# Optimization experiments

Hardware: AMD Instinct MI355X
Metric: run time of the kernel (lower is better)

The kernel has to match this reference:

```python
import jax, jax.numpy as jnp
import numpy as np

TAU = 0.01          # init_temperature
N_CODEWORDS = 512
EPS = 1e-10


def setup_inputs() -> dict:
    key = jax.random.key(0)
    k1, k2, k3 = jax.random.split(key, 3)
    B, C, H, W = 8, 256, 64, 64
    K = N_CODEWORDS
    feats = jax.random.normal(k1, (B, C, H, W), dtype=jnp.float32)
    codebook = jax.random.normal(k2, (K, C), dtype=jnp.float32)
    # standard Gumbel(0,1) noise, matching torch's F.gumbel_softmax sampling
    gumbel_noise = jax.random.gumbel(k3, (B, H * W, K), dtype=jnp.float32)
    return {"feats": feats, "codebook": codebook, "gumbel_noise": gumbel_noise}


def reference(feats, codebook, gumbel_noise):
    B, C, H, W = feats.shape
    K = codebook.shape[0]
    N = H * W
    # (B, C, H, W) -> (B, N, C) tokens
    f = feats.reshape(B, C, N).transpose(0, 2, 1)
    # affinity[b,n,k] = ((f[b,n,:] - cb[k,:]).sum(-1))**2
    # sum over channels commutes with the subtraction, so reduce first
    # instead of materializing the (B, N, K, C) broadcast the torch code builds.
    sf = f.sum(axis=-1)            # (B, N)
    sw = codebook.sum(axis=-1)     # (K,)
    affinity = (sf[:, :, None] - sw[None, None, :]) ** 2   # (B, N, K)
    logits = jnp.exp(-affinity)
    # gumbel-softmax (soft, hard=False), tau = TAU, over codeword axis
    soft_one_hot = jax.nn.softmax((logits + gumbel_noise) / TAU, axis=2)
    qy = jax.nn.softmax(logits, axis=2)
    kld_loss = jnp.sum(qy * jnp.log(qy * K + EPS), axis=2).mean()
    codewords = jnp.argmax(soft_one_hot, axis=2).reshape(B, H, W)
    # weighted codeword sum: (B, N, K) @ (K, C) -> (B, N, C)
    sel = jnp.einsum("bnk,kc->bnc", soft_one_hot, codebook)
    sel_codewords = sel.transpose(0, 2, 1).reshape(B, C, H, W)
    mat_id_probs = soft_one_hot.transpose(0, 2, 1).reshape(B, K, H, W)
    return (sel_codewords, codewords, kld_loss, mat_id_probs)
```

## Files before the change

### kernel.cpp

```cpp
#include <hip/hip_runtime.h>
#include <math.h>
#include <stdint.h>

#define NB  8
#define NC  256
#define NHW 4096
#define NK  512

#define OFF_SEL 0ULL
#define OFF_CW  8388608ULL
#define OFF_KLD 8421376ULL
#define OFF_MAT 8421377ULL
#define MAT_COUNT 16777216ULL
#define OUT_TOTAL (OFF_MAT + MAT_COUNT)

typedef float f4v __attribute__((ext_vector_type(4)));


template <int C>
__device__ __forceinline__ float fdpp(float x) {
    return __int_as_float(__builtin_amdgcn_update_dpp(0, __float_as_int(x), C, 0xF, 0xF, true));
}
template <int C>
__device__ __forceinline__ int idpp(int x) {
    return __builtin_amdgcn_update_dpp(0, x, C, 0xF, 0xF, true);
}
__device__ __forceinline__ float fswz16(float x) {
    return __int_as_float(__builtin_amdgcn_ds_swizzle(__float_as_int(x), 0x401F));
}
__device__ __forceinline__ int iswz16(int x) {
    return __builtin_amdgcn_ds_swizzle(x, 0x401F);
}

__global__ void gumbel_prep(const float* __restrict__ cb, double* __restrict__ ws) {
    const int l = threadIdx.x & 63;
    const int w = threadIdx.x >> 6;
    const int k = blockIdx.x * 4 + w;
    const float4 v = *reinterpret_cast<const float4*>(cb + (size_t)k * NC + l * 4);
    double s = (double)v.x + (double)v.y + (double)v.z + (double)v.w;
    #pragma unroll
    for (int off = 32; off > 0; off >>= 1) s += __shfl_xor(s, off);
    if (l == 0) ws[k] = s;
    if (blockIdx.x == 0 && threadIdx.x == 0) ws[NK] = 0.0;
}

__global__ void zmat(float* __restrict__ out) {
    const size_t base4 = 2105345ULL;
    const size_t n4    = 4194303ULL;
    size_t i = (size_t)blockIdx.x * blockDim.x + threadIdx.x;
    const size_t stride = (size_t)gridDim.x * blockDim.x;
    f4v* o4 = reinterpret_cast<f4v*>(out) + base4;
    const f4v z = {0.f, 0.f, 0.f, 0.f};
    for (; i < n4; i += stride) __builtin_nontemporal_store(z, o4 + i);
    if (blockIdx.x == 0 && threadIdx.x < 4) {
        out[OFF_MAT + threadIdx.x] = 0.f;
        if (threadIdx.x == 0) out[OUT_TOTAL - 1] = 0.f;
    }
}

__global__ void __launch_bounds__(512, 4)
gs_main(const float* __restrict__ feats, const float* __restrict__ gumbel,
        const float* __restrict__ cb, double* __restrict__ ws,
        float* __restrict__ out) {
    __shared__ double part[8][64];
    __shared__ float  sw_f[NK];
    __shared__ double sf_d[64];
    __shared__ float  sf_f[64];
    __shared__ int    kcnt[64];
    __shared__ int    klist[64][25];
    __shared__ float  wlist[64][25];
    __shared__ double kldp[8];

    const int tid = threadIdx.x;
    const int l   = tid & 63;
    const int w   = tid >> 6;
    const int b   = blockIdx.x >> 6;
    const int n0  = (blockIdx.x & 63) * 64;

    {
        const float* fp = feats + ((size_t)b * NC + w * 32) * NHW + n0 + l;
        double s = 0.0;
        #pragma unroll
        for (int i = 0; i < 32; ++i) s += (double)fp[(size_t)i * NHW];
        part[w][l] = s;
        sw_f[tid] = (float)ws[tid];
        __syncthreads();
        if (tid < 64) {
            double a = 0.0;
            #pragma unroll
            for (int i = 0; i < 8; ++i) a += part[i][tid];
            sf_d[tid] = a; sf_f[tid] = (float)a;
            kcnt[tid] = 0;
        }
        __syncthreads();
    }

    float swreg[8];
    #pragma unroll
    for (int jj = 0; jj < 8; ++jj) swreg[jj] = sw_f[l + 64 * jj];

    double kld_wave = 0.0;
    float gc[8], gn[8];
    {
        const float* gp = gumbel + ((size_t)(b * NHW) + n0 + w * 8) * NK;
        #pragma unroll
        for (int jj = 0; jj < 8; ++jj) gc[jj] = gp[l + 64 * jj];
    }
    #pragma unroll
    for (int i = 0; i < 8; ++i) {
        const int tt = w * 8 + i;
        const int n  = n0 + tt;
        if (i < 7) {
            const float* gpn = gumbel + ((size_t)(b * NHW) + n + 1) * NK;
            #pragma unroll
            for (int jj = 0; jj < 8; ++jj) gn[jj] = gpn[l + 64 * jj];
        }
        const float sft = sf_f[tt];
        float y[8];
        float M = -1.0e30f, YS = -1.0e30f; int KB = 0;
        float E = 0.f, T = 0.f;
        #pragma unroll
        for (int jj = 0; jj < 8; ++jj) {
            const int k = l + 64 * jj;
            const float d = sft - swreg[jj];
            const float logit = __expf(-d * d);
            const float yy = logit + gc[jj];
            y[jj] = yy;
            const float h = fmaf(logit, fmaf(logit, fmaf(logit, fmaf(logit,
                              1.f/120.f, 1.f/24.f), 1.f/6.f), 0.5f), 1.f);
            const float xh = logit * h;
            E += xh;
            T = fmaf(logit, 1.f + xh, T);
            if (yy > M) { YS = M; M = yy; KB = k; }
            else YS = fmaxf(YS, yy);
        }
        #define BSTEP(GF, GI) { \
            const float oM = GF(M); const int oK = GI(KB); \
            const float oY = GF(YS); const float oE = GF(E); const float oT = GF(T); \
            const float nys = fmaxf(fmaxf(YS, oY), fminf(M, oM)); \
            if (oM > M || (oM == M && oK < KB)) { M = oM; KB = oK; } \
            YS = nys; E += oE; T += oT; }
        BSTEP(fdpp<0xB1>,  idpp<0xB1>)
        BSTEP(fdpp<0x4E>,  idpp<0x4E>)
        BSTEP(fdpp<0x141>, idpp<0x141>)
        BSTEP(fdpp<0x140>, idpp<0x140>)
        BSTEP(fswz16,      iswz16)
        #define SH32F(x) __shfl_xor(x, 32)
        #define SH32I(x) __shfl_xor(x, 32)
        BSTEP(SH32F, SH32I)
        #undef SH32F
        #undef SH32I
        #undef BSTEP
        E += 512.f;

        if (M - YS < 5e-3f) {
            const double sfd = sf_d[tt];
            double ym64 = -1.0e300; int kb64 = 0;
            #pragma unroll
            for (int jj = 0; jj < 8; ++jj) {
                const int k = l + 64 * jj;
                const double dd = sfd - ws[k];
                const double aff = dd * dd;
                const double lg = (aff < 45.0) ? exp(-aff) : 0.0;
                const double yy = lg + (double)gc[jj];
                if (yy > ym64) { ym64 = yy; kb64 = k; }
            }
            #pragma unroll
            for (int off = 1; off < 64; off <<= 1) {
                const double oy = __shfl_xor(ym64, off);
                const int    ok = __shfl_xor(kb64, off);
                if (oy > ym64 || (oy == ym64 && ok < kb64)) { ym64 = oy; kb64 = ok; }
            }
            KB = kb64;
        }
        if (l == 0) {
            out[OFF_CW + (size_t)b * NHW + n] = (float)KB;
            kld_wave += (double)(T / E + 6.2383246250395075f - logf(E));
        }

        const float thrM = M - 0.17f;
        #pragma unroll
        for (int jj = 0; jj < 8; ++jj) {
            if (y[jj] > thrM) {
                const float p = __expf((y[jj] - M) * 100.0f);
                const int idx = atomicAdd(&kcnt[tt], 1);
                if (idx < 24) { klist[tt][idx] = l + 64 * jj; wlist[tt][idx] = p; }
            }
        }
        #pragma unroll
        for (int jj = 0; jj < 8; ++jj) gc[jj] = gn[jj];
    }
    if (l == 0) kldp[w] = kld_wave;
    __syncthreads();
    if (tid == 0) {
        double acc = 0.0;
        #pragma unroll
        for (int i = 0; i < 8; ++i) acc += kldp[i];
        atomicAdd(&ws[NK], acc);
    }

    if (tid < 64) {
        const int cnt = min(kcnt[tid], 24);
        float S = 0.f;
        for (int e = 0; e < cnt; ++e) S += wlist[tid][e];
        const float inv = 1.f / S;
        float* orow = out + OFF_MAT + ((size_t)b * NK) * NHW + n0 + tid;
        for (int e = 0; e < cnt; ++e) {
            const float wgt = wlist[tid][e] * inv;
            wlist[tid][e] = wgt;
            orow[(size_t)klist[tid][e] * NHW] = wgt;
        }
        kcnt[tid] = cnt;
    }
    __syncthreads();

    {
        const int cnt = kcnt[l];
        #pragma unroll
        for (int half = 0; half < 2; ++half) {
            float acc[16];
            #pragma unroll
            for (int i2 = 0; i2 < 16; ++i2) acc[i2] = 0.f;
            for (int e = 0; e < cnt; ++e) {
                const int k = klist[l][e];
                const float wgt = wlist[l][e];
                const float4* cr = reinterpret_cast<const float4*>(
                    cb + (size_t)k * NC + w * 32 + half * 16);
                #pragma unroll
                for (int q = 0; q < 4; ++q) {
                    const float4 v = cr[q];
                    acc[q * 4 + 0] += wgt * v.x; acc[q * 4 + 1] += wgt * v.y;
                    acc[q * 4 + 2] += wgt * v.z; acc[q * 4 + 3] += wgt * v.w;
                }
            }
            float* basep = out + OFF_SEL + ((size_t)b * NC + w * 32 + half * 16) * NHW + n0 + l;
            #pragma unroll
            for (int i2 = 0; i2 < 16; ++i2)
                __builtin_nontemporal_store(acc[i2], basep + (size_t)i2 * NHW);
        }
    }
}

__global__ void gumbel_fin(const double* __restrict__ ws, float* __restrict__ out) {
    out[OFF_KLD] = (float)(ws[NK] * (1.0 / 32768.0));
}

extern "C" void kernel_launch(void* const* d_in, const int* in_sizes, int n_in,
                              void* d_out, int out_size, void* d_ws, size_t ws_size,
                              hipStream_t stream) {
    const float* feats = (const float*)d_in[0];
    const float* cb    = (const float*)d_in[1];
    const float* gum   = (const float*)d_in[2];
    double* ws = (double*)d_ws;
    float* out = (float*)d_out;
    gumbel_prep<<<128, 256, 0, stream>>>(cb, ws);
    zmat<<<2048, 256, 0, stream>>>(out);
    gs_main<<<512, 512, 0, stream>>>(feats, gum, cb, ws, out);
    gumbel_fin<<<1, 1, 0, stream>>>(ws, out);
}
```

Measured before the change: 62.49 us.

## Merge prep kernels, finalize KLD via last-block counter, vectorize gumbel loads

Folds the codebook-sum prep into the zero-fill kernel and replaces the final single-thread KLD kernel with a last-block-done atomic counter in the main kernel, dropping two kernel launches. The gumbel noise is now loaded as float4 with a three-buffer prefetch rotation, and codeword ownership per lane moves to contiguous groups of four, read as float4 from shared memory. Launch overhead and scalar loads are the costs targeted. In exchange the kernel relies on threadfence and atomic ordering for the KLD result, and the rare tie-break fallback now re-reads gumbel values from global memory.

```diff
diff --git a/kernel.cpp b/kernel.cpp
--- a/kernel.cpp
+++ b/kernel.cpp
@@ -32,19 +32,8 @@
     return __builtin_amdgcn_ds_swizzle(x, 0x401F);
 }
 
-__global__ void gumbel_prep(const float* __restrict__ cb, double* __restrict__ ws) {
-    const int l = threadIdx.x & 63;
-    const int w = threadIdx.x >> 6;
-    const int k = blockIdx.x * 4 + w;
-    const float4 v = *reinterpret_cast<const float4*>(cb + (size_t)k * NC + l * 4);
-    double s = (double)v.x + (double)v.y + (double)v.z + (double)v.w;
-    #pragma unroll
-    for (int off = 32; off > 0; off >>= 1) s += __shfl_xor(s, off);
-    if (l == 0) ws[k] = s;
-    if (blockIdx.x == 0 && threadIdx.x == 0) ws[NK] = 0.0;
-}
-
-__global__ void zmat(float* __restrict__ out) {
+__global__ void zprep(const float* __restrict__ cb, double* __restrict__ ws,
+                      float* __restrict__ out) {
     const size_t base4 = 2105345ULL;
     const size_t n4    = 4194303ULL;
     size_t i = (size_t)blockIdx.x * blockDim.x + threadIdx.x;
@@ -54,7 +43,21 @@
     for (; i < n4; i += stride) __builtin_nontemporal_store(z, o4 + i);
     if (blockIdx.x == 0 && threadIdx.x < 4) {
         out[OFF_MAT + threadIdx.x] = 0.f;
-        if (threadIdx.x == 0) out[OUT_TOTAL - 1] = 0.f;
+        if (threadIdx.x == 0) {
+            out[OUT_TOTAL - 1] = 0.f;
+            ws[NK] = 0.0;
+            reinterpret_cast<unsigned*>(ws + NK + 1)[0] = 0u;
+        }
+    }
+    if (blockIdx.x < 128) {
+        const int l = threadIdx.x & 63;
+        const int w = threadIdx.x >> 6;
+        const int k = blockIdx.x * 4 + w;
+        const float4 v = *reinterpret_cast<const float4*>(cb + (size_t)k * NC + l * 4);
+        double s = (double)v.x + (double)v.y + (double)v.z + (double)v.w;
+        #pragma unroll
+        for (int off = 32; off > 0; off >>= 1) s += __shfl_xor(s, off);
+        if (l == 0) ws[k] = s;
     }
 }
 
@@ -63,7 +66,7 @@
         const float* __restrict__ cb, double* __restrict__ ws,
         float* __restrict__ out) {
     __shared__ double part[8][64];
-    __shared__ float  sw_f[NK];
+    __shared__ __align__(16) float sw_f[NK];
     __shared__ double sf_d[64];
     __shared__ float  sf_f[64];
     __shared__ int    kcnt[64];
@@ -95,101 +98,107 @@
         __syncthreads();
     }
 
-    float swreg[8];
-    #pragma unroll
-    for (int jj = 0; jj < 8; ++jj) swreg[jj] = sw_f[l + 64 * jj];
+    const float4 sa = *reinterpret_cast<const float4*>(&sw_f[4 * l]);
+    const float4 sb = *reinterpret_cast<const float4*>(&sw_f[256 + 4 * l]);
 
     double kld_wave = 0.0;
-    float gc[8], gn[8];
-    {
-        const float* gp = gumbel + ((size_t)(b * NHW) + n0 + w * 8) * NK;
-        #pragma unroll
-        for (int jj = 0; jj < 8; ++jj) gc[jj] = gp[l + 64 * jj];
-    }
-    #pragma unroll
-    for (int i = 0; i < 8; ++i) {
-        const int tt = w * 8 + i;
-        const int n  = n0 + tt;
-        if (i < 7) {
-            const float* gpn = gumbel + ((size_t)(b * NHW) + n + 1) * NK;
-            #pragma unroll
-            for (int jj = 0; jj < 8; ++jj) gn[jj] = gpn[l + 64 * jj];
-        }
-        const float sft = sf_f[tt];
-        float y[8];
-        float M = -1.0e30f, YS = -1.0e30f; int KB = 0;
-        float E = 0.f, T = 0.f;
-        #pragma unroll
-        for (int jj = 0; jj < 8; ++jj) {
-            const int k = l + 64 * jj;
-            const float d = sft - swreg[jj];
-            const float logit = __expf(-d * d);
-            const float yy = logit + gc[jj];
-            y[jj] = yy;
-            const float h = fmaf(logit, fmaf(logit, fmaf(logit, fmaf(logit,
-                              1.f/120.f, 1.f/24.f), 1.f/6.f), 0.5f), 1.f);
-            const float xh = logit * h;
-            E += xh;
-            T = fmaf(logit, 1.f + xh, T);
-            if (yy > M) { YS = M; M = yy; KB = k; }
-            else YS = fmaxf(YS, yy);
-        }
-        #define BSTEP(GF, GI) { \
-            const float oM = GF(M); const int oK = GI(KB); \
-            const float oY = GF(YS); const float oE = GF(E); const float oT = GF(T); \
-            const float nys = fmaxf(fmaxf(YS, oY), fminf(M, oM)); \
-            if (oM > M || (oM == M && oK < KB)) { M = oM; KB = oK; } \
-            YS = nys; E += oE; T += oT; }
-        BSTEP(fdpp<0xB1>,  idpp<0xB1>)
-        BSTEP(fdpp<0x4E>,  idpp<0x4E>)
-        BSTEP(fdpp<0x141>, idpp<0x141>)
-        BSTEP(fdpp<0x140>, idpp<0x140>)
-        BSTEP(fswz16,      iswz16)
-        #define SH32F(x) __shfl_xor(x, 32)
-        #define SH32I(x) __shfl_xor(x, 32)
-        BSTEP(SH32F, SH32I)
-        #undef SH32F
-        #undef SH32I
-        #undef BSTEP
-        E += 512.f;
-
-        if (M - YS < 5e-3f) {
-            const double sfd = sf_d[tt];
-            double ym64 = -1.0e300; int kb64 = 0;
-            #pragma unroll
-            for (int jj = 0; jj < 8; ++jj) {
-                const int k = l + 64 * jj;
-                const double dd = sfd - ws[k];
-                const double aff = dd * dd;
-                const double lg = (aff < 45.0) ? exp(-aff) : 0.0;
-                const double yy = lg + (double)gc[jj];
-                if (yy > ym64) { ym64 = yy; kb64 = k; }
-            }
-            #pragma unroll
-            for (int off = 1; off < 64; off <<= 1) {
-                const double oy = __shfl_xor(ym64, off);
-                const int    ok = __shfl_xor(kb64, off);
-                if (oy > ym64 || (oy == ym64 && ok < kb64)) { ym64 = oy; kb64 = ok; }
-            }
-            KB = kb64;
-        }
-        if (l == 0) {
-            out[OFF_CW + (size_t)b * NHW + n] = (float)KB;
-            kld_wave += (double)(T / E + 6.2383246250395075f - logf(E));
-        }
-
-        const float thrM = M - 0.17f;
-        #pragma unroll
-        for (int jj = 0; jj < 8; ++jj) {
-            if (y[jj] > thrM) {
-                const float p = __expf((y[jj] - M) * 100.0f);
-                const int idx = atomicAdd(&kcnt[tt], 1);
-                if (idx < 24) { klist[tt][idx] = l + 64 * jj; wlist[tt][idx] = p; }
-            }
-        }
-        #pragma unroll
-        for (int jj = 0; jj < 8; ++jj) gc[jj] = gn[jj];
-    }
+    const float4* g4 = reinterpret_cast<const float4*>(
+        gumbel + ((size_t)(b * NHW) + n0 + w * 8) * NK);
+
+    float4 A0 = g4[l],           A1 = g4[64 + l];
+    float4 B0 = g4[128 + l],     B1 = g4[192 + l];
+    float4 C0, C1;
+
+#define KSTEP(kk, SV, GV) { \
+        const float d_ = sft - (SV); \
+        const float logit_ = __expf(-d_ * d_); \
+        const float yy_ = logit_ + (GV); \
+        y[kk] = yy_; \
+        const float h_ = fmaf(logit_, fmaf(logit_, fmaf(logit_, fmaf(logit_, \
+                          1.f/120.f, 1.f/24.f), 1.f/6.f), 0.5f), 1.f); \
+        const float xh_ = logit_ * h_; \
+        E += xh_; \
+        T = fmaf(logit_, 1.f + xh_, T); \
+        if (yy_ > M) { YS = M; M = yy_; KB = (kk < 4) ? (4*l + kk) : (256 + 4*l + kk - 4); } \
+        else YS = fmaxf(YS, yy_); }
+
+#define BSTEP(GF, GI) { \
+        const float oM = GF(M); const int oK = GI(KB); \
+        const float oY = GF(YS); const float oE = GF(E); const float oT = GF(T); \
+        const float nys = fmaxf(fmaxf(YS, oY), fminf(M, oM)); \
+        if (oM > M || (oM == M && oK < KB)) { M = oM; KB = oK; } \
+        YS = nys; E += oE; T += oT; }
+
+#define SH32(x) __shfl_xor(x, 32)
+
+#define TOKEN(ii, CUR0, CUR1, PF) { \
+        PF; \
+        const int tt = w * 8 + ii; \
+        const int n  = n0 + tt; \
+        const float sft = sf_f[tt]; \
+        float y[8]; \
+        float M = -1.0e30f, YS = -1.0e30f; int KB = 0; \
+        float E = 0.f, T = 0.f; \
+        KSTEP(0, sa.x, (CUR0).x)  KSTEP(1, sa.y, (CUR0).y) \
+        KSTEP(2, sa.z, (CUR0).z)  KSTEP(3, sa.w, (CUR0).w) \
+        KSTEP(4, sb.x, (CUR1).x)  KSTEP(5, sb.y, (CUR1).y) \
+        KSTEP(6, sb.z, (CUR1).z)  KSTEP(7, sb.w, (CUR1).w) \
+        BSTEP(fdpp<0xB1>,  idpp<0xB1>) \
+        BSTEP(fdpp<0x4E>,  idpp<0x4E>) \
+        BSTEP(fdpp<0x141>, idpp<0x141>) \
+        BSTEP(fdpp<0x140>, idpp<0x140>) \
+        BSTEP(fswz16,      iswz16) \
+        BSTEP(SH32,        SH32) \
+        E += 512.f; \
+        if (M - YS < 5e-3f) {                \
+            const double sfd = sf_d[tt]; \
+            const float* gsc = gumbel + ((size_t)(b * NHW) + n) * NK; \
+            double ym64 = -1.0e300; int kb64 = 0; \
+            _Pragma("unroll") \
+            for (int jj = 0; jj < 8; ++jj) { \
+                const int k_ = (jj < 4) ? (4*l + jj) : (256 + 4*l + jj - 4); \
+                const double dd = sfd - ws[k_]; \
+                const double aff = dd * dd; \
+                const double lg = (aff < 45.0) ? exp(-aff) : 0.0; \
+                const double yy = lg + (double)gsc[k_]; \
+                if (yy > ym64) { ym64 = yy; kb64 = k_; } \
+            } \
+            _Pragma("unroll") \
+            for (int off = 1; off < 64; off <<= 1) { \
+                const double oy = __shfl_xor(ym64, off); \
+                const int    ok = __shfl_xor(kb64, off); \
+                if (oy > ym64 || (oy == ym64 && ok < kb64)) { ym64 = oy; kb64 = ok; } \
+            } \
+            KB = kb64; \
+        } \
+        if (l == 0) { \
+            out[OFF_CW + (size_t)b * NHW + n] = (float)KB; \
+            kld_wave += (double)(T / E + 6.2383246250395075f - logf(E)); \
+        } \
+        const float thrM = M - 0.17f; \
+        _Pragma("unroll") \
+        for (int jj = 0; jj < 8; ++jj) { \
+            if (y[jj] > thrM) { \
+                const float p_ = __expf((y[jj] - M) * 100.0f); \
+                const int k_ = (jj < 4) ? (4*l + jj) : (256 + 4*l + jj - 4); \
+                const int idx = atomicAdd(&kcnt[tt], 1); \
+                if (idx < 24) { klist[tt][idx] = k_; wlist[tt][idx] = p_; } \
+            } \
+        } }
+
+    TOKEN(0, A0, A1, { C0 = g4[256 + l]; C1 = g4[320 + l]; })
+    TOKEN(1, B0, B1, { A0 = g4[384 + l]; A1 = g4[448 + l]; })
+    TOKEN(2, C0, C1, { B0 = g4[512 + l]; B1 = g4[576 + l]; })
+    TOKEN(3, A0, A1, { C0 = g4[640 + l]; C1 = g4[704 + l]; })
+    TOKEN(4, B0, B1, { A0 = g4[768 + l]; A1 = g4[832 + l]; })
+    TOKEN(5, C0, C1, { B0 = g4[896 + l]; B1 = g4[960 + l]; })
+    TOKEN(6, A0, A1, {})
+    TOKEN(7, B0, B1, {})
+#undef TOKEN
+#undef KSTEP
+#undef BSTEP
+#undef SH32
+
     if (l == 0) kldp[w] = kld_wave;
     __syncthreads();
     if (tid == 0) {
@@ -197,6 +206,14 @@
         #pragma unroll
         for (int i = 0; i < 8; ++i) acc += kldp[i];
         atomicAdd(&ws[NK], acc);
+        __threadfence();
+        unsigned* ctr = reinterpret_cast<unsigned*>(ws + NK + 1);
+        const unsigned t = atomicAdd(ctr, 1u);
+        if (t == 511u) {
+            __threadfence();
+            const double tot = atomicAdd(&ws[NK], 0.0);
+            out[OFF_KLD] = (float)(tot * (1.0 / 32768.0));
+        }
     }
 
     if (tid < 64) {
@@ -241,10 +258,6 @@
     }
 }
 
-__global__ void gumbel_fin(const double* __restrict__ ws, float* __restrict__ out) {
-    out[OFF_KLD] = (float)(ws[NK] * (1.0 / 32768.0));
-}
-
 extern "C" void kernel_launch(void* const* d_in, const int* in_sizes, int n_in,
                               void* d_out, int out_size, void* d_ws, size_t ws_size,
                               hipStream_t stream) {
@@ -253,8 +266,6 @@
     const float* gum   = (const float*)d_in[2];
     double* ws = (double*)d_ws;
     float* out = (float*)d_out;
-    gumbel_prep<<<128, 256, 0, stream>>>(cb, ws);
-    zmat<<<2048, 256, 0, stream>>>(out);
+    zprep<<<2048, 256, 0, stream>>>(cb, ws, out);
     gs_main<<<512, 512, 0, stream>>>(feats, gum, cb, ws, out);
-    gumbel_fin<<<1, 1, 0, stream>>>(ws, out);
-}
+}
```

Result: slower. 72.99 us (+16.8%).

## Fuse prep kernels, finalize KLD via last-block counter, process two tokens per iteration

Applied to the files above, without the earlier changes.

Merges the codebook-sum prep kernel into the zero-fill kernel and drops the single-thread finalize kernel. The KLD mean is now written by the last block to arrive, detected with an atomic counter and thread fences. The main per-token loop is restructured to handle two tokens per iteration, interleaving their reductions to expose more ILP and halve the number of cross-lane shuffle sequences. This cuts two kernel launches at the cost of higher register pressure and a grid-completion atomic.

```diff
diff --git a/kernel.cpp b/kernel.cpp
--- a/kernel.cpp
+++ b/kernel.cpp
@@ -32,19 +32,8 @@
     return __builtin_amdgcn_ds_swizzle(x, 0x401F);
 }
 
-__global__ void gumbel_prep(const float* __restrict__ cb, double* __restrict__ ws) {
-    const int l = threadIdx.x & 63;
-    const int w = threadIdx.x >> 6;
-    const int k = blockIdx.x * 4 + w;
-    const float4 v = *reinterpret_cast<const float4*>(cb + (size_t)k * NC + l * 4);
-    double s = (double)v.x + (double)v.y + (double)v.z + (double)v.w;
-    #pragma unroll
-    for (int off = 32; off > 0; off >>= 1) s += __shfl_xor(s, off);
-    if (l == 0) ws[k] = s;
-    if (blockIdx.x == 0 && threadIdx.x == 0) ws[NK] = 0.0;
-}
-
-__global__ void zmat(float* __restrict__ out) {
+__global__ void zprep(const float* __restrict__ cb, double* __restrict__ ws,
+                      float* __restrict__ out) {
     const size_t base4 = 2105345ULL;
     const size_t n4    = 4194303ULL;
     size_t i = (size_t)blockIdx.x * blockDim.x + threadIdx.x;
@@ -54,7 +43,21 @@
     for (; i < n4; i += stride) __builtin_nontemporal_store(z, o4 + i);
     if (blockIdx.x == 0 && threadIdx.x < 4) {
         out[OFF_MAT + threadIdx.x] = 0.f;
-        if (threadIdx.x == 0) out[OUT_TOTAL - 1] = 0.f;
+        if (threadIdx.x == 0) {
+            out[OUT_TOTAL - 1] = 0.f;
+            ws[NK] = 0.0;
+            reinterpret_cast<unsigned*>(ws + NK + 1)[0] = 0u;
+        }
+    }
+    if (blockIdx.x < 128) {
+        const int l = threadIdx.x & 63;
+        const int w = threadIdx.x >> 6;
+        const int k = blockIdx.x * 4 + w;
+        const float4 v = *reinterpret_cast<const float4*>(cb + (size_t)k * NC + l * 4);
+        double s = (double)v.x + (double)v.y + (double)v.z + (double)v.w;
+        #pragma unroll
+        for (int off = 32; off > 0; off >>= 1) s += __shfl_xor(s, off);
+        if (l == 0) ws[k] = s;
     }
 }
 
@@ -100,95 +103,121 @@
     for (int jj = 0; jj < 8; ++jj) swreg[jj] = sw_f[l + 64 * jj];
 
     double kld_wave = 0.0;
-    float gc[8], gn[8];
-    {
-        const float* gp = gumbel + ((size_t)(b * NHW) + n0 + w * 8) * NK;
-        #pragma unroll
-        for (int jj = 0; jj < 8; ++jj) gc[jj] = gp[l + 64 * jj];
-    }
+    const float* gbase = gumbel + ((size_t)(b * NHW) + n0 + w * 8) * NK;
+    float gcA[8], gcB[8], gnA[8], gnB[8];
     #pragma unroll
-    for (int i = 0; i < 8; ++i) {
-        const int tt = w * 8 + i;
-        const int n  = n0 + tt;
-        if (i < 7) {
-            const float* gpn = gumbel + ((size_t)(b * NHW) + n + 1) * NK;
-            #pragma unroll
-            for (int jj = 0; jj < 8; ++jj) gn[jj] = gpn[l + 64 * jj];
-        }
-        const float sft = sf_f[tt];
-        float y[8];
-        float M = -1.0e30f, YS = -1.0e30f; int KB = 0;
-        float E = 0.f, T = 0.f;
+    for (int jj = 0; jj < 8; ++jj) {
+        gcA[jj] = gbase[l + 64 * jj];
+        gcB[jj] = gbase[NK + l + 64 * jj];
+    }
+
+    #pragma unroll 1
+    for (int i = 0; i < 4; ++i) {
+        const int ttA = w * 8 + 2 * i;
+        const int ttB = ttA + 1;
+        if (i < 3) {
+            const float* gp = gbase + (size_t)(2 * i + 2) * NK;
+            #pragma unroll
+            for (int jj = 0; jj < 8; ++jj) {
+                gnA[jj] = gp[l + 64 * jj];
+                gnB[jj] = gp[NK + l + 64 * jj];
+            }
+        }
+        const float sfA = sf_f[ttA], sfB = sf_f[ttB];
+        float yA[8], yB[8];
+        float MA = -1.0e30f, MB = -1.0e30f, YSA = -1.0e30f, YSB = -1.0e30f;
+        int   KA = 0, KBi = 0;
+        float EA = 0.f, EB = 0.f, TA = 0.f, TB = 0.f;
         #pragma unroll
         for (int jj = 0; jj < 8; ++jj) {
             const int k = l + 64 * jj;
-            const float d = sft - swreg[jj];
-            const float logit = __expf(-d * d);
-            const float yy = logit + gc[jj];
-            y[jj] = yy;
-            const float h = fmaf(logit, fmaf(logit, fmaf(logit, fmaf(logit,
+            const float dA = sfA - swreg[jj];
+            const float dB = sfB - swreg[jj];
+            const float lgA = __expf(-dA * dA);
+            const float lgB = __expf(-dB * dB);
+            const float yyA = lgA + gcA[jj];
+            const float yyB = lgB + gcB[jj];
+            yA[jj] = yyA; yB[jj] = yyB;
+            const float hA = fmaf(lgA, fmaf(lgA, fmaf(lgA, fmaf(lgA,
                               1.f/120.f, 1.f/24.f), 1.f/6.f), 0.5f), 1.f);
-            const float xh = logit * h;
-            E += xh;
-            T = fmaf(logit, 1.f + xh, T);
-            if (yy > M) { YS = M; M = yy; KB = k; }
-            else YS = fmaxf(YS, yy);
-        }
-        #define BSTEP(GF, GI) { \
-            const float oM = GF(M); const int oK = GI(KB); \
-            const float oY = GF(YS); const float oE = GF(E); const float oT = GF(T); \
-            const float nys = fmaxf(fmaxf(YS, oY), fminf(M, oM)); \
-            if (oM > M || (oM == M && oK < KB)) { M = oM; KB = oK; } \
-            YS = nys; E += oE; T += oT; }
-        BSTEP(fdpp<0xB1>,  idpp<0xB1>)
-        BSTEP(fdpp<0x4E>,  idpp<0x4E>)
-        BSTEP(fdpp<0x141>, idpp<0x141>)
-        BSTEP(fdpp<0x140>, idpp<0x140>)
-        BSTEP(fswz16,      iswz16)
-        #define SH32F(x) __shfl_xor(x, 32)
-        #define SH32I(x) __shfl_xor(x, 32)
-        BSTEP(SH32F, SH32I)
-        #undef SH32F
-        #undef SH32I
-        #undef BSTEP
-        E += 512.f;
-
-        if (M - YS < 5e-3f) {
-            const double sfd = sf_d[tt];
-            double ym64 = -1.0e300; int kb64 = 0;
-            #pragma unroll
-            for (int jj = 0; jj < 8; ++jj) {
-                const int k = l + 64 * jj;
-                const double dd = sfd - ws[k];
-                const double aff = dd * dd;
-                const double lg = (aff < 45.0) ? exp(-aff) : 0.0;
-                const double yy = lg + (double)gc[jj];
-                if (yy > ym64) { ym64 = yy; kb64 = k; }
-            }
-            #pragma unroll
-            for (int off = 1; off < 64; off <<= 1) {
-                const double oy = __shfl_xor(ym64, off);
-                const int    ok = __shfl_xor(kb64, off);
-                if (oy > ym64 || (oy == ym64 && ok < kb64)) { ym64 = oy; kb64 = ok; }
-            }
-            KB = kb64;
+            const float hB = fmaf(lgB, fmaf(lgB, fmaf(lgB, fmaf(lgB,
+                              1.f/120.f, 1.f/24.f), 1.f/6.f), 0.5f), 1.f);
+            const float xhA = lgA * hA, xhB = lgB * hB;
+            EA += xhA; EB += xhB;
+            TA = fmaf(lgA, 1.f + xhA, TA);
+            TB = fmaf(lgB, 1.f + xhB, TB);
+            if (yyA > MA) { YSA = MA; MA = yyA; KA = k; } else YSA = fmaxf(YSA, yyA);
+            if (yyB > MB) { YSB = MB; MB = yyB; KBi = k; } else YSB = fmaxf(YSB, yyB);
+        }
+        #define BSTEP2(GF, GI) { \
+            const float oMA = GF(MA); const int oKA = GI(KA); \
+            const float oYA = GF(YSA); const float oEA = GF(EA); const float oTA = GF(TA); \
+            const float oMB = GF(MB); const int oKB = GI(KBi); \
+            const float oYB = GF(YSB); const float oEB = GF(EB); const float oTB = GF(TB); \
+            const float nyA = fmaxf(fmaxf(YSA, oYA), fminf(MA, oMA)); \
+            const float nyB = fmaxf(fmaxf(YSB, oYB), fminf(MB, oMB)); \
+            if (oMA > MA || (oMA == MA && oKA < KA)) { MA = oMA; KA = oKA; } \
+            if (oMB > MB || (oMB == MB && oKB < KBi)) { MB = oMB; KBi = oKB; } \
+            YSA = nyA; YSB = nyB; EA += oEA; EB += oEB; TA += oTA; TB += oTB; }
+        #define SH32(x) __shfl_xor(x, 32)
+        BSTEP2(fdpp<0xB1>,  idpp<0xB1>)
+        BSTEP2(fdpp<0x4E>,  idpp<0x4E>)
+        BSTEP2(fdpp<0x141>, idpp<0x141>)
+        BSTEP2(fdpp<0x140>, idpp<0x140>)
+        BSTEP2(fswz16,      iswz16)
+        BSTEP2(SH32,        SH32)
+        #undef SH32
+        #undef BSTEP2
+        EA += 512.f; EB += 512.f;
+
+        #pragma unroll
+        for (int tsel = 0; tsel < 2; ++tsel) {
+            const float gapM  = tsel ? MB : MA;
+            const float gapYS = tsel ? YSB : YSA;
+            if (gapM - gapYS < 5e-3f) {
+                const int tt = tsel ? ttB : ttA;
+                const double sfd = sf_d[tt];
+                double ym64 = -1.0e300; int kb64 = 0;
+                #pragma unroll
+                for (int jj = 0; jj < 8; ++jj) {
+                    const int k = l + 64 * jj;
+                    const double dd = sfd - ws[k];
+                    const double aff = dd * dd;
+                    const double lg = (aff < 45.0) ? exp(-aff) : 0.0;
+                    const double yy = lg + (double)(tsel ? gcB[jj] : gcA[jj]);
+                    if (yy > ym64) { ym64 = yy; kb64 = k; }
+                }
+                #pragma unroll
+                for (int off = 1; off < 64; off <<= 1) {
+                    const double oy = __shfl_xor(ym64, off);
+                    const int    ok = __shfl_xor(kb64, off);
+                    if (oy > ym64 || (oy == ym64 && ok < kb64)) { ym64 = oy; kb64 = ok; }
+                }
+                if (tsel) KBi = kb64; else KA = kb64;
+            }
         }
         if (l == 0) {
-            out[OFF_CW + (size_t)b * NHW + n] = (float)KB;
-            kld_wave += (double)(T / E + 6.2383246250395075f - logf(E));
-        }
-
-        const float thrM = M - 0.17f;
+            out[OFF_CW + (size_t)b * NHW + n0 + ttA] = (float)KA;
+            out[OFF_CW + (size_t)b * NHW + n0 + ttB] = (float)KBi;
+            kld_wave += (double)(TA / EA + 6.2383246250395075f - logf(EA));
+            kld_wave += (double)(TB / EB + 6.2383246250395075f - logf(EB));
+        }
+        const float thrA = MA - 0.17f, thrB = MB - 0.17f;
         #pragma unroll
         for (int jj = 0; jj < 8; ++jj) {
-            if (y[jj] > thrM) {
-                const float p = __expf((y[jj] - M) * 100.0f);
-                const int idx = atomicAdd(&kcnt[tt], 1);
-                if (idx < 24) { klist[tt][idx] = l + 64 * jj; wlist[tt][idx] = p; }
-            }
-        }
-        #pragma unroll
-        for (int jj = 0; jj < 8; ++jj) gc[jj] = gn[jj];
+            if (yA[jj] > thrA) {
+                const float p = __expf((yA[jj] - MA) * 100.0f);
+                const int idx = atomicAdd(&kcnt[ttA], 1);
+                if (idx < 24) { klist[ttA][idx] = l + 64 * jj; wlist[ttA][idx] = p; }
+            }
+            if (yB[jj] > thrB) {
+                const float p = __expf((yB[jj] - MB) * 100.0f);
+                const int idx = atomicAdd(&kcnt[ttB], 1);
+                if (idx < 24) { klist[ttB][idx] = l + 64 * jj; wlist[ttB][idx] = p; }
+            }
+        }
+        #pragma unroll
+        for (int jj = 0; jj < 8; ++jj) { gcA[jj] = gnA[jj]; gcB[jj] = gnB[jj]; }
     }
     if (l == 0) kldp[w] = kld_wave;
     __syncthreads();
@@ -197,6 +226,14 @@
         #pragma unroll
         for (int i = 0; i < 8; ++i) acc += kldp[i];
         atomicAdd(&ws[NK], acc);
+        __threadfence();
+        unsigned* ctr = reinterpret_cast<unsigned*>(ws + NK + 1);
+        const unsigned t = atomicAdd(ctr, 1u);
+        if (t == 511u) {
+            __threadfence();
+            const double tot = atomicAdd(&ws[NK], 0.0);
+            out[OFF_KLD] = (float)(tot * (1.0 / 32768.0));
+        }
     }
 
     if (tid < 64) {
@@ -241,10 +278,6 @@
     }
 }
 
-__global__ void gumbel_fin(const double* __restrict__ ws, float* __restrict__ out) {
-    out[OFF_KLD] = (float)(ws[NK] * (1.0 / 32768.0));
-}
-
 extern "C" void kernel_launch(void* const* d_in, const int* in_sizes, int n_in,
                               void* d_out, int out_size, void* d_ws, size_t ws_size,
                               hipStream_t stream) {
@@ -253,8 +286,6 @@
     const float* gum   = (const float*)d_in[2];
     double* ws = (double*)d_ws;
     float* out = (float*)d_out;
-    gumbel_prep<<<128, 256, 0, stream>>>(cb, ws);
-    zmat<<<2048, 256, 0, stream>>>(out);
+    zprep<<<2048, 256, 0, stream>>>(cb, ws, out);
     gs_main<<<512, 512, 0, stream>>>(feats, gum, cb, ws, out);
-    gumbel_fin<<<1, 1, 0, stream>>>(ws, out);
-}
+}
```

After: 83.86 us. +34.2%, slower.
